# Performance work log

Hardware: AMD Instinct MI355X
Metric: run time of the kernel (lower is better)

The kernel has to match this reference:

```python
import jax, jax.numpy as jnp
import numpy as np

B, S, H, P = 16, 8192, 512, 32

def setup_inputs() -> dict:
    key = jax.random.key(0)
    k1, k2 = jax.random.split(key)
    birnn_outputs = jax.random.normal(k1, (B, S, H), dtype=jnp.float32)
    self_attn = jax.random.normal(k2, (P, H), dtype=jnp.float32)
    return {"birnn_outputs": birnn_outputs, "self_attn": self_attn}

def reference(birnn_outputs, self_attn):
    # scores: [B, P, S] = probes [P,H] x birnn_outputs^T [B,H,S]
    scores = jnp.einsum('ph,bsh->bps', self_attn, birnn_outputs)
    attn = jax.nn.softmax(scores, axis=-1)  # softmax over seq_len
    # context: [B, P, H]
    ctx = jnp.einsum('bps,bsh->bph', attn, birnn_outputs)
    return ctx.reshape(ctx.shape[0], -1)  # [B, P*H]
```

## Files before the change

kernel.cpp:

```cpp
#include <hip/hip_runtime.h>
#include <hip/hip_bf16.h>

#define BB 16
#define SS 8192
#define HH 512
#define PP 32
#define NC 32
#define CH 256

typedef __attribute__((ext_vector_type(8))) short short8;
typedef __attribute__((ext_vector_type(4))) float f32x4;

__device__ inline unsigned short bf16_hi_trunc(float x) {
  union { float f; unsigned u; } v; v.f = x;
  return (unsigned short)(v.u >> 16);
}
__device__ inline unsigned short bf16_rne(float x) {
  union { float f; unsigned u; } v; v.f = x;
  unsigned r = v.u + 0x7FFFu + ((v.u >> 16) & 1u);
  return (unsigned short)(r >> 16);
}
__device__ inline float from_hi(unsigned short h) {
  union { unsigned u; float f; } v; v.u = ((unsigned)h) << 16;
  return v.f;
}
__device__ inline f32x4 max4(f32x4 a, f32x4 b) {
  f32x4 r; r.x = fmaxf(a.x, b.x); r.y = fmaxf(a.y, b.y);
  r.z = fmaxf(a.z, b.z); r.w = fmaxf(a.w, b.w); return r;
}
__device__ inline f32x4 exp4(f32x4 a) {
  f32x4 r; r.x = __expf(a.x); r.y = __expf(a.y);
  r.z = __expf(a.z); r.w = __expf(a.w); return r;
}
__device__ inline f32x4 fma_b(float a, f32x4 b, f32x4 c) {
  c.x = fmaf(a, b.x, c.x); c.y = fmaf(a, b.y, c.y);
  c.z = fmaf(a, b.z, c.z); c.w = fmaf(a, b.w, c.w); return c;
}
__device__ inline void cvt8(const float* xv, short8& bh, short8& bl) {
#pragma unroll
  for (int j = 0; j < 8; ++j) {
    unsigned short h = bf16_hi_trunc(xv[j]);
    bh[j] = (short)h;
    bl[j] = (short)bf16_rne(xv[j] - from_hi(h));
  }
}

__global__ void k_prep(const float* __restrict__ probes,
                       short* __restrict__ Ph, short* __restrict__ Pl) {
  int t = threadIdx.x;
  for (int q = t; q < 2048; q += 256) {
    int lane = q & 63, kcg = (q >> 6) & 15, nt = q >> 10;
    int p = nt * 16 + (lane & 15);
    int h0 = kcg * 32 + (lane >> 4) * 8;
#pragma unroll
    for (int j = 0; j < 8; ++j) {
      float f = probes[p * HH + h0 + j];
      unsigned short h = bf16_hi_trunc(f);
      Ph[q * 8 + j] = (short)h;
      Pl[q * 8 + j] = (short)bf16_rne(f - from_hi(h));
    }
  }
}

__global__ __launch_bounds__(512, 4) void k_fused(
    const float* __restrict__ x, const short* __restrict__ Ph,
    const short* __restrict__ Pl, float* __restrict__ pm,
    float* __restrict__ pl_, float* __restrict__ part) {
  __shared__ float sc_[CH][36];
  __shared__ f32x4 sm[64][8];
  __shared__ f32x4 sl[64][8];
  __shared__ f32x4 mS4[8];

  const int t = threadIdx.x;
  const int lane = t & 63, w = t >> 6;
  const int scnk = blockIdx.x;
  const int b = blockIdx.y;
  const size_t xbase = ((size_t)b * SS + (size_t)scnk * CH) * HH;

#pragma unroll
  for (int tile = 0; tile < CH / 128; ++tile) {
    f32x4 acc0 = (f32x4){0.f, 0.f, 0.f, 0.f};
    f32x4 acc1 = (f32x4){0.f, 0.f, 0.f, 0.f};
    const int rl = tile * 128 + w * 16 + (lane & 15);
    const float* xr = x + xbase + (size_t)rl * HH + (lane >> 4) * 8;
#pragma unroll 2
    for (int kcg = 0; kcg < 16; ++kcg) {
      f32x4 xa = *(const f32x4*)(xr + kcg * 32);
      f32x4 xc = *(const f32x4*)(xr + kcg * 32 + 4);
      float xv[8] = {xa.x, xa.y, xa.z, xa.w, xc.x, xc.y, xc.z, xc.w};
      short8 xh, xl;
      cvt8(xv, xh, xl);
      short8 ph0 = *(const short8*)(Ph + ((size_t)(kcg * 64 + lane)) * 8);
      short8 pl0 = *(const short8*)(Pl + ((size_t)(kcg * 64 + lane)) * 8);
      short8 ph1 = *(const short8*)(Ph + ((size_t)((16 + kcg) * 64 + lane)) * 8);
      short8 pl1 = *(const short8*)(Pl + ((size_t)((16 + kcg) * 64 + lane)) * 8);
      acc0 = __builtin_amdgcn_mfma_f32_16x16x32_bf16(xh, ph0, acc0, 0, 0, 0);
      acc0 = __builtin_amdgcn_mfma_f32_16x16x32_bf16(xh, pl0, acc0, 0, 0, 0);
      acc0 = __builtin_amdgcn_mfma_f32_16x16x32_bf16(xl, ph0, acc0, 0, 0, 0);
      acc1 = __builtin_amdgcn_mfma_f32_16x16x32_bf16(xh, ph1, acc1, 0, 0, 0);
      acc1 = __builtin_amdgcn_mfma_f32_16x16x32_bf16(xh, pl1, acc1, 0, 0, 0);
      acc1 = __builtin_amdgcn_mfma_f32_16x16x32_bf16(xl, ph1, acc1, 0, 0, 0);
    }
#pragma unroll
    for (int r = 0; r < 4; ++r) {
      int s_ = tile * 128 + w * 16 + (lane >> 4) * 4 + r;
      sc_[s_][lane & 15] = acc0[r];
      sc_[s_][16 + (lane & 15)] = acc1[r];
    }
  }
  __syncthreads();

  {
    const int p4 = t & 7, sg = t >> 3;
    f32x4 m4 = (f32x4){-1e30f, -1e30f, -1e30f, -1e30f};
    f32x4 l4 = (f32x4){0.f, 0.f, 0.f, 0.f};
#pragma unroll
    for (int i = 0; i < CH / 64; ++i) {
      int s_ = sg + 64 * i;
      f32x4 v = *(const f32x4*)&sc_[s_][p4 * 4];
      f32x4 nm = max4(m4, v);
      l4 = l4 * exp4(m4 - nm) + exp4(v - nm);
      m4 = nm;
    }
    sm[sg][p4] = m4;
    sl[sg][p4] = l4;
  }
  __syncthreads();
  if (t < 8) {
    f32x4 M = sm[0][t], L = sl[0][t];
#pragma unroll
    for (int i = 1; i < 64; ++i) {
      f32x4 m2 = sm[i][t], l2 = sl[i][t];
      f32x4 nm = max4(M, m2);
      L = L * exp4(M - nm) + l2 * exp4(m2 - nm);
      M = nm;
    }
    mS4[t] = M;
    *(f32x4*)&pm[(size_t)(b * NC + scnk) * PP + t * 4] = M;
    *(f32x4*)&pl_[(size_t)(b * NC + scnk) * PP + t * 4] = L;
  }
  __syncthreads();

  {
    const float* mSf = (const float*)mS4;
#pragma unroll
    for (int i = 0; i < CH * PP / 512; ++i) {
      int idx = t + 512 * i;
      int s_ = idx >> 5, p = idx & 31;
      sc_[s_][p] = __expf(sc_[s_][p] - mSf[p]);
    }
  }
  __syncthreads();

  const float* xrow = x + xbase + lane * 8;
  f32x4 acc[4][2];
#pragma unroll
  for (int pi = 0; pi < 4; ++pi) {
    acc[pi][0] = (f32x4){0.f, 0.f, 0.f, 0.f};
    acc[pi][1] = (f32x4){0.f, 0.f, 0.f, 0.f};
  }
  for (int jo = 0; jo < CH; jo += 4) {
    f32x4 xv0[4], xv1[4];
#pragma unroll
    for (int u = 0; u < 4; ++u) {
      const float* xp = xrow + (size_t)(jo + u) * HH;
      xv0[u] = *(const f32x4*)xp;
      xv1[u] = *(const f32x4*)(xp + 4);
    }
#pragma unroll
    for (int u = 0; u < 4; ++u) {
      f32x4 w0 = *(const f32x4*)&sc_[jo + u][w * 4];
      acc[0][0] = fma_b(w0.x, xv0[u], acc[0][0]);
      acc[0][1] = fma_b(w0.x, xv1[u], acc[0][1]);
      acc[1][0] = fma_b(w0.y, xv0[u], acc[1][0]);
      acc[1][1] = fma_b(w0.y, xv1[u], acc[1][1]);
      acc[2][0] = fma_b(w0.z, xv0[u], acc[2][0]);
      acc[2][1] = fma_b(w0.z, xv1[u], acc[2][1]);
      acc[3][0] = fma_b(w0.w, xv0[u], acc[3][0]);
      acc[3][1] = fma_b(w0.w, xv1[u], acc[3][1]);
    }
  }
#pragma unroll
  for (int pi = 0; pi < 4; ++pi) {
    int p = w * 4 + pi;
    float* o = part + (((size_t)scnk * BB + b) * PP + p) * HH + lane * 8;
    *(f32x4*)o = acc[pi][0];
    *(f32x4*)(o + 4) = acc[pi][1];
  }
}

__global__ __launch_bounds__(256) void k_merge(
    const float* __restrict__ part, const float* __restrict__ pm,
    const float* __restrict__ pl_, float* __restrict__ out) {
  const int bp = blockIdx.x;
  const int b = bp >> 5, p = bp & 31;
  const int t = threadIdx.x;

  float M = -1e30f;
#pragma unroll
  for (int c = 0; c < NC; ++c)
    M = fmaxf(M, pm[(size_t)(b * NC + c) * PP + p]);
  float f[NC];
  float L = 0.f;
#pragma unroll
  for (int c = 0; c < NC; ++c) {
    float e = __expf(pm[(size_t)(b * NC + c) * PP + p] - M);
    f[c] = e;
    L += pl_[(size_t)(b * NC + c) * PP + p] * e;
  }
  const float inv = 1.f / L;

  float sx = 0.f, sy = 0.f;
#pragma unroll
  for (int c = 0; c < NC; ++c) {
    const float* q = part + (((size_t)c * BB + b) * PP + p) * HH + t * 2;
    sx = fmaf(q[0], f[c], sx);
    sy = fmaf(q[1], f[c], sy);
  }
  float* o = out + (size_t)bp * HH + t * 2;
  o[0] = sx * inv;
  o[1] = sy * inv;
}

extern "C" void kernel_launch(void* const* d_in, const int* in_sizes, int n_in,
                              void* d_out, int out_size, void* d_ws, size_t ws_size,
                              hipStream_t stream) {
  const float* x = (const float*)d_in[0];
  const float* probes = (const float*)d_in[1];
  float* out = (float*)d_out;

  float* part = (float*)d_ws;
  float* pm = part + (size_t)NC * BB * PP * HH;
  float* pl_ = pm + BB * NC * PP;
  short* Ph = (short*)(pl_ + BB * NC * PP);
  short* Pl = Ph + PP * HH;

  k_prep<<<1, 256, 0, stream>>>(probes, Ph, Pl);
  k_fused<<<dim3(NC, BB), 512, 0, stream>>>(x, Ph, Pl, pm, pl_, part);
  k_merge<<<dim3(BB * PP), 256, 0, stream>>>(part, pm, pl_, out);
}
```

Before: 483.6 us.

## Stage second-pass x rows through LDS with async double-buffered global_load_lds

The weighted-sum pass no longer has every wave load the same x rows from global memory. The block now cooperatively streams 8-row stages into a double-buffered LDS pool using global_load_lds, prefetching the next stage while the current one is consumed. The pool reuses the space of the softmax reduction scratch, and the score-loop unroll goes from 2 to 4. This adds two barriers per stage and about 32KB of LDS per block, which may reduce occupancy. The final iteration issues a redundant prefetch of stage 0.

Measured after the change: 463.2 us. 1.04x faster.

```diff
diff --git a/kernel.cpp b/kernel.cpp
--- a/kernel.cpp
+++ b/kernel.cpp
@@ -43,6 +43,11 @@
     bh[j] = (short)h;
     bl[j] = (short)bf16_rne(xv[j] - from_hi(h));
   }
+}
+__device__ inline void gll16(const float* g, float* l) {
+  __builtin_amdgcn_global_load_lds(
+      (const __attribute__((address_space(1))) unsigned int*)g,
+      (__attribute__((address_space(3))) unsigned int*)l, 16, 0, 0);
 }
 
 __global__ void k_prep(const float* __restrict__ probes,
@@ -67,9 +72,7 @@
     const short* __restrict__ Pl, float* __restrict__ pm,
     float* __restrict__ pl_, float* __restrict__ part) {
   __shared__ float sc_[CH][36];
-  __shared__ f32x4 sm[64][8];
-  __shared__ f32x4 sl[64][8];
-  __shared__ f32x4 mS4[8];
+  __shared__ f32x4 pool4[2048];
 
   const int t = threadIdx.x;
   const int lane = t & 63, w = t >> 6;
@@ -83,7 +86,7 @@
     f32x4 acc1 = (f32x4){0.f, 0.f, 0.f, 0.f};
     const int rl = tile * 128 + w * 16 + (lane & 15);
     const float* xr = x + xbase + (size_t)rl * HH + (lane >> 4) * 8;
-#pragma unroll 2
+#pragma unroll 4
     for (int kcg = 0; kcg < 16; ++kcg) {
       f32x4 xa = *(const f32x4*)(xr + kcg * 32);
       f32x4 xc = *(const f32x4*)(xr + kcg * 32 + 4);
@@ -110,6 +113,9 @@
   }
   __syncthreads();
 
+  f32x4 (*sm)[8] = reinterpret_cast<f32x4(*)[8]>(pool4);
+  f32x4 (*sl)[8] = reinterpret_cast<f32x4(*)[8]>(pool4 + 512);
+  f32x4* mS4 = pool4 + 1024;
   {
     const int p4 = t & 7, sg = t >> 3;
     f32x4 m4 = (f32x4){-1e30f, -1e30f, -1e30f, -1e30f};
@@ -152,34 +158,48 @@
   }
   __syncthreads();
 
-  const float* xrow = x + xbase + lane * 8;
+  float* xs = (float*)pool4;
+  const float* xg = x + xbase;
+  const int so = w * 512 + lane * 4;
+  const int do_ = w * 512;
+
   f32x4 acc[4][2];
 #pragma unroll
   for (int pi = 0; pi < 4; ++pi) {
     acc[pi][0] = (f32x4){0.f, 0.f, 0.f, 0.f};
     acc[pi][1] = (f32x4){0.f, 0.f, 0.f, 0.f};
   }
-  for (int jo = 0; jo < CH; jo += 4) {
-    f32x4 xv0[4], xv1[4];
-#pragma unroll
-    for (int u = 0; u < 4; ++u) {
-      const float* xp = xrow + (size_t)(jo + u) * HH;
-      xv0[u] = *(const f32x4*)xp;
-      xv1[u] = *(const f32x4*)(xp + 4);
-    }
-#pragma unroll
-    for (int u = 0; u < 4; ++u) {
-      f32x4 w0 = *(const f32x4*)&sc_[jo + u][w * 4];
-      acc[0][0] = fma_b(w0.x, xv0[u], acc[0][0]);
-      acc[0][1] = fma_b(w0.x, xv1[u], acc[0][1]);
-      acc[1][0] = fma_b(w0.y, xv0[u], acc[1][0]);
-      acc[1][1] = fma_b(w0.y, xv1[u], acc[1][1]);
-      acc[2][0] = fma_b(w0.z, xv0[u], acc[2][0]);
-      acc[2][1] = fma_b(w0.z, xv1[u], acc[2][1]);
-      acc[3][0] = fma_b(w0.w, xv0[u], acc[3][0]);
-      acc[3][1] = fma_b(w0.w, xv1[u], acc[3][1]);
-    }
-  }
+
+  gll16(xg + so, xs + do_);
+  gll16(xg + so + 256, xs + do_ + 256);
+
+  for (int st = 0; st < 32; ++st) {
+    const int nst = (st + 1) & 31;
+    const int nbuf = (st + 1) & 1;
+    gll16(xg + (size_t)nst * 4096 + so, xs + nbuf * 4096 + do_);
+    gll16(xg + (size_t)nst * 4096 + so + 256, xs + nbuf * 4096 + do_ + 256);
+    asm volatile("s_waitcnt vmcnt(2)" ::: "memory");
+    __builtin_amdgcn_s_barrier();
+    __builtin_amdgcn_sched_barrier(0);
+    const float* xb = xs + (st & 1) * 4096;
+#pragma unroll
+    for (int j = 0; j < 8; ++j) {
+      f32x4 xv0 = *(const f32x4*)(xb + j * 512 + lane * 8);
+      f32x4 xv1 = *(const f32x4*)(xb + j * 512 + lane * 8 + 4);
+      f32x4 w0 = *(const f32x4*)&sc_[st * 8 + j][w * 4];
+      acc[0][0] = fma_b(w0.x, xv0, acc[0][0]);
+      acc[0][1] = fma_b(w0.x, xv1, acc[0][1]);
+      acc[1][0] = fma_b(w0.y, xv0, acc[1][0]);
+      acc[1][1] = fma_b(w0.y, xv1, acc[1][1]);
+      acc[2][0] = fma_b(w0.z, xv0, acc[2][0]);
+      acc[2][1] = fma_b(w0.z, xv1, acc[2][1]);
+      acc[3][0] = fma_b(w0.w, xv0, acc[3][0]);
+      acc[3][1] = fma_b(w0.w, xv1, acc[3][1]);
+    }
+    __builtin_amdgcn_sched_barrier(0);
+    __builtin_amdgcn_s_barrier();
+  }
+
 #pragma unroll
   for (int pi = 0; pi < 4; ++pi) {
     int p = w * 4 + pi;
```
